# Optimization experiments

Hardware: AMD Instinct MI355X
Metric: run time of the kernel (lower is better)

Reference implementation:

```python
import jax, jax.numpy as jnp
import numpy as np

LAYER_NUMS = 3
# activations per layer: elu, elu, none (matches expert_activations=["elu","elu",null])
ACTS = [jax.nn.elu, jax.nn.elu, None]


def setup_inputs() -> dict:
    key = jax.random.key(0)
    k1, k2, k3, k4 = jax.random.split(key, 4)
    E, D, B_ = 8, 2048, 4096
    weight_blend = jax.random.uniform(k1, (E,), dtype=jnp.float32)
    x = jax.random.normal(k2, (B_, D), dtype=jnp.float32)
    W = jax.random.normal(k3, (LAYER_NUMS, E, D, D), dtype=jnp.float32) * 0.02
    B = jax.random.normal(k4, (LAYER_NUMS, D), dtype=jnp.float32) * 0.02
    return {"weight_blend": weight_blend, "x": x, "W": W, "B": B}


def reference(weight_blend, x, W, B):
    # Dropout is identity in eval/deterministic mode (expert_keep_prob=0.0).
    for i in range(LAYER_NUMS):
        # blended weight: sum_e c_e * W_e  -> (out, in)
        w = jnp.einsum("e,eoi->oi", weight_blend, W[i])
        x = x @ w.T + B[i]
        if ACTS[i] is not None:
            x = ACTS[i](x)
    return x
```

## Files before the change

kernel.cpp:

```cpp
#include <hip/hip_runtime.h>
#include <hip/hip_bf16.h>

#define MDIM 4096
#define NDIM 2048
#define KDIM 2048
#define KTILES 32
#define PER_LAYER 4194304

typedef __attribute__((ext_vector_type(8))) short bf16x8;
typedef __attribute__((ext_vector_type(4))) float f32x4;

__device__ __forceinline__ unsigned short f2bf(float f) {
    unsigned u = __builtin_bit_cast(unsigned, f);
    u += 0x7FFFu + ((u >> 16) & 1u);
    return (unsigned short)(u >> 16);
}

__global__ __launch_bounds__(256) void blend0_kernel(
    const float* __restrict__ W, const float* __restrict__ cb,
    const float* __restrict__ x,
    unsigned short* __restrict__ wb, unsigned short* __restrict__ xb)
{
    float c[8];
#pragma unroll
    for (int e = 0; e < 8; ++e) c[e] = cb[e];
    const unsigned wtotal4 = PER_LAYER >> 2;
    const unsigned xtotal4 = 2097152u;
    const unsigned total = wtotal4 + xtotal4;
    unsigned stride = gridDim.x * blockDim.x;
    for (unsigned i = blockIdx.x * blockDim.x + threadIdx.x; i < total; i += stride) {
        if (i < wtotal4) {
            unsigned off = i << 2;
            const float* base = W + off;
            float4 s = make_float4(0.f, 0.f, 0.f, 0.f);
#pragma unroll
            for (int e = 0; e < 8; ++e) {
                float4 v = *(const float4*)(base + (size_t)e * PER_LAYER);
                s.x += c[e] * v.x; s.y += c[e] * v.y;
                s.z += c[e] * v.z; s.w += c[e] * v.w;
            }
            ushort4 o;
            o.x = f2bf(s.x); o.y = f2bf(s.y); o.z = f2bf(s.z); o.w = f2bf(s.w);
            *(ushort4*)(wb + off) = o;
        } else {
            unsigned j = (i - wtotal4) << 2;
            float4 v = *(const float4*)(x + j);
            ushort4 o;
            o.x = f2bf(v.x); o.y = f2bf(v.y); o.z = f2bf(v.z); o.w = f2bf(v.w);
            *(ushort4*)(xb + j) = o;
        }
    }
}

#define BARR() do { asm volatile("" ::: "memory"); __builtin_amdgcn_s_barrier(); asm volatile("" ::: "memory"); } while (0)
#define SP(N) __builtin_amdgcn_s_setprio(N)
#define VMC_IMPL(N) asm volatile("s_waitcnt vmcnt(" #N ")" ::: "memory")
#define VMC(N) VMC_IMPL(N)

template<int ACT, typename OutT, int BLEND>
__global__ __launch_bounds__(512, 2) void gemm_fused(
    const unsigned short* __restrict__ A,
    const unsigned short* __restrict__ Bw,
    const float* __restrict__ bias,
    OutT* __restrict__ C,
    const float* __restrict__ Wnext,
    const float* __restrict__ cb,
    unsigned short* __restrict__ wbNext)
{
    __shared__ __align__(16) unsigned short lds[73728];
    char* ldsc = (char*)lds;

    const int tid = threadIdx.x;
    const int wid = tid >> 6;
    const int lane = tid & 63;
    const int wr = wid >> 1;
    const int wc = wid & 1;

    float cw[8];
    if (BLEND) {
#pragma unroll
        for (int e = 0; e < 8; ++e) cw[e] = cb[e];
        VMC(0);
    }

    const int wg = (blockIdx.x & 7) * 32 + (blockIdx.x >> 3);
    const size_t blockM = (size_t)(wg & 15) * 256;
    const size_t blockN = (size_t)(wg >> 4) * 128;

    const int sw = (lane & 7) << 4;
    const int ck = (lane >> 4) << 4;
    const int rAb = wr * 64 + (lane & 15);
    const int rBb = wc * 64 + (lane & 15);

    const int srow = tid >> 3;
    const int scol = ((tid & 7) ^ (srow & 7)) << 3;
    const unsigned short* aStage = A + (blockM + srow) * KDIM + scol;
    const unsigned short* bStage = Bw + (blockN + srow) * KDIM + scol;

#define STAGE_AS(BUF, S, KT) do { \
    const unsigned short* g_ = aStage + (size_t)(S) * 64 * KDIM + (size_t)(KT) * 64; \
    __builtin_amdgcn_global_load_lds((const __attribute__((address_space(1))) void*)g_, \
        (__attribute__((address_space(3))) void*)(ldsc + (BUF) * 49152 + (S) * 8192 + tid * 16), \
        16, 0, 0); \
} while (0)

#define STAGE_BS(BUF, S, KT) do { \
    const unsigned short* g_ = bStage + (size_t)(S) * 64 * KDIM + (size_t)(KT) * 64; \
    __builtin_amdgcn_global_load_lds((const __attribute__((address_space(1))) void*)g_, \
        (__attribute__((address_space(3))) void*)(ldsc + (BUF) * 49152 + 32768 + (S) * 8192 + tid * 16), \
        16, 0, 0); \
} while (0)

#define RD_A(BUF, M, KK) \
    (*(const bf16x8*)(ldsc + (BUF) * 49152 + ((rAb + (M) * 16)) * 128 + (((KK) * 64 + ck) ^ sw)))
#define RD_B(BUF, N, KK) \
    (*(const bf16x8*)(ldsc + (BUF) * 49152 + 32768 + (rBb + (N) * 16) * 128 + (((KK) * 64 + ck) ^ sw)))

    f32x4 acc[4][4];
#pragma unroll
    for (int m = 0; m < 4; ++m)
#pragma unroll
        for (int n = 0; n < 4; ++n) acc[m][n] = (f32x4){0.f, 0.f, 0.f, 0.f};

#define GEMM_ITER(T, WAITER) do { \
    int stb_ = cur + 2; if (stb_ >= 3) stb_ -= 3; \
    bf16x8 af[4][2], bfr[4][2]; \
    _Pragma("unroll") for (int m_ = 0; m_ < 4; ++m_) { \
        af[m_][0] = RD_A(cur, m_, 0); af[m_][1] = RD_A(cur, m_, 1); } \
    _Pragma("unroll") for (int n_ = 0; n_ < 4; ++n_) { \
        bfr[n_][0] = RD_B(cur, n_, 0); bfr[n_][1] = RD_B(cur, n_, 1); } \
    if ((T) + 2 < KTILES) { \
        STAGE_AS(stb_, 0, (T) + 2); STAGE_AS(stb_, 1, (T) + 2); \
        STAGE_AS(stb_, 2, (T) + 2); STAGE_AS(stb_, 3, (T) + 2); \
        STAGE_BS(stb_, 0, (T) + 2); STAGE_BS(stb_, 1, (T) + 2); \
    } \
    SP(1); \
    _Pragma("unroll") for (int kk_ = 0; kk_ < 2; ++kk_) \
    _Pragma("unroll") for (int m_ = 0; m_ < 4; ++m_) \
    _Pragma("unroll") for (int n_ = 0; n_ < 4; ++n_) \
        acc[m_][n_] = __builtin_amdgcn_mfma_f32_16x16x32_bf16( \
            af[m_][kk_], bfr[n_][kk_], acc[m_][n_], 0, 0, 0); \
    SP(0); \
    WAITER; \
    BARR(); \
    cur = cur + 1; if (cur >= 3) cur = 0; \
} while (0)

#define BLEND_STEP(G) do { \
    const unsigned idx_ = (unsigned)(G) * 131072u + (unsigned)blockIdx.x * 512u + (unsigned)tid; \
    const unsigned off_ = idx_ << 2; \
    const float* bs_ = Wnext + off_; \
    float4 s_ = make_float4(0.f, 0.f, 0.f, 0.f); \
    _Pragma("unroll") for (int e_ = 0; e_ < 8; ++e_) { \
        float4 v_ = *(const float4*)(bs_ + (size_t)e_ * PER_LAYER); \
        s_.x += cw[e_] * v_.x; s_.y += cw[e_] * v_.y; \
        s_.z += cw[e_] * v_.z; s_.w += cw[e_] * v_.w; } \
    ushort4 o_; \
    o_.x = f2bf(s_.x); o_.y = f2bf(s_.y); o_.z = f2bf(s_.z); o_.w = f2bf(s_.w); \
    *(ushort4*)(wbNext + off_) = o_; \
} while (0)

    STAGE_AS(0, 0, 0); STAGE_AS(0, 1, 0); STAGE_AS(0, 2, 0); STAGE_AS(0, 3, 0);
    STAGE_BS(0, 0, 0); STAGE_BS(0, 1, 0);
    STAGE_AS(1, 0, 1); STAGE_AS(1, 1, 1); STAGE_AS(1, 2, 1); STAGE_AS(1, 3, 1);
    STAGE_BS(1, 0, 1); STAGE_BS(1, 1, 1);
    VMC(6);
    BARR();

    int cur = 0;
    if (BLEND) {
#pragma unroll 1
        for (int g = 0; g < 8; ++g) {
            const int t0 = 3 * g;
            GEMM_ITER(t0, VMC(6));
            BLEND_STEP(g);
            GEMM_ITER(t0 + 1, VMC(15));
            GEMM_ITER(t0 + 2, VMC(6));
        }
#pragma unroll 1
        for (int t = 24; t < 30; ++t) GEMM_ITER(t, VMC(6));
    } else {
#pragma unroll 1
        for (int t = 0; t < 30; ++t) GEMM_ITER(t, VMC(6));
    }
    GEMM_ITER(30, VMC(0));
    GEMM_ITER(31, VMC(0));

    const int crow = (lane >> 4) * 4;
    const int ccol = lane & 15;
#pragma unroll
    for (int m = 0; m < 4; ++m)
#pragma unroll
        for (int n = 0; n < 4; ++n) {
            const size_t col = blockN + wc * 64 + n * 16 + ccol;
            const float bv = bias[col];
#pragma unroll
            for (int r = 0; r < 4; ++r) {
                const size_t row = blockM + wr * 64 + m * 16 + crow + r;
                float v = acc[m][n][r] + bv;
                if (ACT) v = v > 0.f ? v : expm1f(v);
                if constexpr (sizeof(OutT) == 2) {
                    C[row * NDIM + col] = (OutT)f2bf(v);
                } else {
                    C[row * NDIM + col] = (OutT)v;
                }
            }
        }
#undef STAGE_AS
#undef STAGE_BS
#undef RD_A
#undef RD_B
#undef GEMM_ITER
#undef BLEND_STEP
}

extern "C" void kernel_launch(void* const* d_in, const int* in_sizes, int n_in,
                              void* d_out, int out_size, void* d_ws, size_t ws_size,
                              hipStream_t stream) {
    const float* blendw = (const float*)d_in[0];
    const float* x      = (const float*)d_in[1];
    const float* W      = (const float*)d_in[2];
    const float* Bb     = (const float*)d_in[3];
    float* out = (float*)d_out;

    unsigned short* wb0 = (unsigned short*)d_ws;
    unsigned short* wb1 = wb0 + PER_LAYER;
    unsigned short* wb2 = wb1 + PER_LAYER;
    unsigned short* xb  = wb2 + PER_LAYER;
    unsigned short* y0  = xb + 8388608;
    unsigned short* y1  = xb;

    blend0_kernel<<<2048, 256, 0, stream>>>(W, blendw, x, wb0, xb);

    gemm_fused<1, unsigned short, 1><<<256, 512, 0, stream>>>(
        xb, wb0, Bb,        y0,  W + (size_t)8 * PER_LAYER,  blendw, wb1);
    gemm_fused<1, unsigned short, 1><<<256, 512, 0, stream>>>(
        y0, wb1, Bb + 2048, y1,  W + (size_t)16 * PER_LAYER, blendw, wb2);
    gemm_fused<0, float, 0><<<256, 512, 0, stream>>>(
        y1, wb2, Bb + 4096, out, nullptr, nullptr, nullptr);
}
```

Baseline: 204.8 us.

## Shrink GEMM tiles to 128x128 with 256 threads and double buffering

```diff
diff --git a/kernel.cpp b/kernel.cpp
--- a/kernel.cpp
+++ b/kernel.cpp
@@ -58,7 +58,7 @@
 #define VMC(N) VMC_IMPL(N)
 
 template<int ACT, typename OutT, int BLEND>
-__global__ __launch_bounds__(512, 2) void gemm_fused(
+__global__ __launch_bounds__(256, 2) void gemm_fused(
     const unsigned short* __restrict__ A,
     const unsigned short* __restrict__ Bw,
     const float* __restrict__ bias,
@@ -67,7 +67,7 @@
     const float* __restrict__ cb,
     unsigned short* __restrict__ wbNext)
 {
-    __shared__ __align__(16) unsigned short lds[73728];
+    __shared__ __align__(16) unsigned short lds[32768];
     char* ldsc = (char*)lds;
 
     const int tid = threadIdx.x;
@@ -83,9 +83,10 @@
         VMC(0);
     }
 
-    const int wg = (blockIdx.x & 7) * 32 + (blockIdx.x >> 3);
-    const size_t blockM = (size_t)(wg & 15) * 256;
-    const size_t blockN = (size_t)(wg >> 4) * 128;
+    const int k8 = blockIdx.x & 7;
+    const int j = blockIdx.x >> 3;
+    const size_t blockM = (size_t)((k8 & 3) * 8 + (j >> 3)) * 128;
+    const size_t blockN = (size_t)((k8 >> 2) * 8 + (j & 7)) * 128;
 
     const int sw = (lane & 7) << 4;
     const int ck = (lane >> 4) << 4;
@@ -97,24 +98,25 @@
     const unsigned short* aStage = A + (blockM + srow) * KDIM + scol;
     const unsigned short* bStage = Bw + (blockN + srow) * KDIM + scol;
 
-#define STAGE_AS(BUF, S, KT) do { \
-    const unsigned short* g_ = aStage + (size_t)(S) * 64 * KDIM + (size_t)(KT) * 64; \
-    __builtin_amdgcn_global_load_lds((const __attribute__((address_space(1))) void*)g_, \
-        (__attribute__((address_space(3))) void*)(ldsc + (BUF) * 49152 + (S) * 8192 + tid * 16), \
-        16, 0, 0); \
+#define STAGE_TILE(BUF, KT) do { \
+    _Pragma("unroll") for (int s_ = 0; s_ < 4; ++s_) { \
+        const unsigned short* ga_ = aStage + (size_t)s_ * 32 * KDIM + (size_t)(KT) * 64; \
+        __builtin_amdgcn_global_load_lds((const __attribute__((address_space(1))) void*)ga_, \
+            (__attribute__((address_space(3))) void*)(ldsc + (BUF) * 32768 + s_ * 4096 + tid * 16), \
+            16, 0, 0); \
+    } \
+    _Pragma("unroll") for (int s_ = 0; s_ < 4; ++s_) { \
+        const unsigned short* gb_ = bStage + (size_t)s_ * 32 * KDIM + (size_t)(KT) * 64; \
+        __builtin_amdgcn_global_load_lds((const __attribute__((address_space(1))) void*)gb_, \
+            (__attribute__((address_space(3))) void*)(ldsc + (BUF) * 32768 + 16384 + s_ * 4096 + tid * 16), \
+            16, 0, 0); \
+    } \
 } while (0)
 
-#define STAGE_BS(BUF, S, KT) do { \
-    const unsigned short* g_ = bStage + (size_t)(S) * 64 * KDIM + (size_t)(KT) * 64; \
-    __builtin_amdgcn_global_load_lds((const __attribute__((address_space(1))) void*)g_, \
-        (__attribute__((address_space(3))) void*)(ldsc + (BUF) * 49152 + 32768 + (S) * 8192 + tid * 16), \
-        16, 0, 0); \
-} while (0)
-
 #define RD_A(BUF, M, KK) \
-    (*(const bf16x8*)(ldsc + (BUF) * 49152 + ((rAb + (M) * 16)) * 128 + (((KK) * 64 + ck) ^ sw)))
+    (*(const bf16x8*)(ldsc + (BUF) * 32768 + (rAb + (M) * 16) * 128 + (((KK) * 64 + ck) ^ sw)))
 #define RD_B(BUF, N, KK) \
-    (*(const bf16x8*)(ldsc + (BUF) * 49152 + 32768 + (rBb + (N) * 16) * 128 + (((KK) * 64 + ck) ^ sw)))
+    (*(const bf16x8*)(ldsc + (BUF) * 32768 + 16384 + (rBb + (N) * 16) * 128 + (((KK) * 64 + ck) ^ sw)))
 
     f32x4 acc[4][4];
 #pragma unroll
@@ -122,32 +124,8 @@
 #pragma unroll
         for (int n = 0; n < 4; ++n) acc[m][n] = (f32x4){0.f, 0.f, 0.f, 0.f};
 
-#define GEMM_ITER(T, WAITER) do { \
-    int stb_ = cur + 2; if (stb_ >= 3) stb_ -= 3; \
-    bf16x8 af[4][2], bfr[4][2]; \
-    _Pragma("unroll") for (int m_ = 0; m_ < 4; ++m_) { \
-        af[m_][0] = RD_A(cur, m_, 0); af[m_][1] = RD_A(cur, m_, 1); } \
-    _Pragma("unroll") for (int n_ = 0; n_ < 4; ++n_) { \
-        bfr[n_][0] = RD_B(cur, n_, 0); bfr[n_][1] = RD_B(cur, n_, 1); } \
-    if ((T) + 2 < KTILES) { \
-        STAGE_AS(stb_, 0, (T) + 2); STAGE_AS(stb_, 1, (T) + 2); \
-        STAGE_AS(stb_, 2, (T) + 2); STAGE_AS(stb_, 3, (T) + 2); \
-        STAGE_BS(stb_, 0, (T) + 2); STAGE_BS(stb_, 1, (T) + 2); \
-    } \
-    SP(1); \
-    _Pragma("unroll") for (int kk_ = 0; kk_ < 2; ++kk_) \
-    _Pragma("unroll") for (int m_ = 0; m_ < 4; ++m_) \
-    _Pragma("unroll") for (int n_ = 0; n_ < 4; ++n_) \
-        acc[m_][n_] = __builtin_amdgcn_mfma_f32_16x16x32_bf16( \
-            af[m_][kk_], bfr[n_][kk_], acc[m_][n_], 0, 0, 0); \
-    SP(0); \
-    WAITER; \
-    BARR(); \
-    cur = cur + 1; if (cur >= 3) cur = 0; \
-} while (0)
-
 #define BLEND_STEP(G) do { \
-    const unsigned idx_ = (unsigned)(G) * 131072u + (unsigned)blockIdx.x * 512u + (unsigned)tid; \
+    const unsigned idx_ = (unsigned)(G) * 131072u + (unsigned)blockIdx.x * 256u + (unsigned)tid; \
     const unsigned off_ = idx_ << 2; \
     const float* bs_ = Wnext + off_; \
     float4 s_ = make_float4(0.f, 0.f, 0.f, 0.f); \
@@ -160,31 +138,34 @@
     *(ushort4*)(wbNext + off_) = o_; \
 } while (0)
 
-    STAGE_AS(0, 0, 0); STAGE_AS(0, 1, 0); STAGE_AS(0, 2, 0); STAGE_AS(0, 3, 0);
-    STAGE_BS(0, 0, 0); STAGE_BS(0, 1, 0);
-    STAGE_AS(1, 0, 1); STAGE_AS(1, 1, 1); STAGE_AS(1, 2, 1); STAGE_AS(1, 3, 1);
-    STAGE_BS(1, 0, 1); STAGE_BS(1, 1, 1);
-    VMC(6);
+    STAGE_TILE(0, 0);
+    STAGE_TILE(1, 1);
+    VMC(8);
     BARR();
 
-    int cur = 0;
-    if (BLEND) {
 #pragma unroll 1
-        for (int g = 0; g < 8; ++g) {
-            const int t0 = 3 * g;
-            GEMM_ITER(t0, VMC(6));
-            BLEND_STEP(g);
-            GEMM_ITER(t0 + 1, VMC(15));
-            GEMM_ITER(t0 + 2, VMC(6));
-        }
-#pragma unroll 1
-        for (int t = 24; t < 30; ++t) GEMM_ITER(t, VMC(6));
-    } else {
-#pragma unroll 1
-        for (int t = 0; t < 30; ++t) GEMM_ITER(t, VMC(6));
+    for (int t = 0; t < KTILES; ++t) {
+        const int cur = t & 1;
+        bf16x8 af[4][2], bfr[4][2];
+#pragma unroll
+        for (int m = 0; m < 4; ++m) { af[m][0] = RD_A(cur, m, 0); af[m][1] = RD_A(cur, m, 1); }
+#pragma unroll
+        for (int n = 0; n < 4; ++n) { bfr[n][0] = RD_B(cur, n, 0); bfr[n][1] = RD_B(cur, n, 1); }
+        if (t >= 1 && t + 1 < KTILES) STAGE_TILE(cur ^ 1, t + 1);
+        if (BLEND && (t & 3) == 0) BLEND_STEP(t >> 2);
+        SP(1);
+#pragma unroll
+        for (int kk = 0; kk < 2; ++kk)
+#pragma unroll
+            for (int m = 0; m < 4; ++m)
+#pragma unroll
+                for (int n = 0; n < 4; ++n)
+                    acc[m][n] = __builtin_amdgcn_mfma_f32_16x16x32_bf16(
+                        af[m][kk], bfr[n][kk], acc[m][n], 0, 0, 0);
+        SP(0);
+        VMC(0);
+        BARR();
     }
-    GEMM_ITER(30, VMC(0));
-    GEMM_ITER(31, VMC(0));
 
     const int crow = (lane >> 4) * 4;
     const int ccol = lane & 15;
@@ -206,11 +187,9 @@
                 }
             }
         }
-#undef STAGE_AS
-#undef STAGE_BS
+#undef STAGE_TILE
 #undef RD_A
 #undef RD_B
-#undef GEMM_ITER
 #undef BLEND_STEP
 }
 
@@ -232,10 +211,11 @@
 
     blend0_kernel<<<2048, 256, 0, stream>>>(W, blendw, x, wb0, xb);
 
-    gemm_fused<1, unsigned short, 1><<<256, 512, 0, stream>>>(
+    const int grid = (MDIM / 128) * (NDIM / 128);
+    gemm_fused<1, unsigned short, 1><<<grid, 256, 0, stream>>>(
         xb, wb0, Bb,        y0,  W + (size_t)8 * PER_LAYER,  blendw, wb1);
-    gemm_fused<1, unsigned short, 1><<<256, 512, 0, stream>>>(
+    gemm_fused<1, unsigned short, 1><<<grid, 256, 0, stream>>>(
         y0, wb1, Bb + 2048, y1,  W + (size_t)16 * PER_LAYER, blendw, wb2);
-    gemm_fused<0, float, 0><<<256, 512, 0, stream>>>(
+    gemm_fused<0, float, 0><<<grid, 256, 0, stream>>>(
         y1, wb2, Bb + 4096, out, nullptr, nullptr, nullptr);
 }
```

Result: no change. 206.0 us (+0.6%).

## Split GEMM iteration into quadrant phases interleaving LDS reads, staging and MFMA

Applied to the files above, without the earlier changes.

```diff
diff --git a/kernel.cpp b/kernel.cpp
--- a/kernel.cpp
+++ b/kernel.cpp
@@ -54,6 +54,7 @@
 
 #define BARR() do { asm volatile("" ::: "memory"); __builtin_amdgcn_s_barrier(); asm volatile("" ::: "memory"); } while (0)
 #define SP(N) __builtin_amdgcn_s_setprio(N)
+#define LGKM0() asm volatile("s_waitcnt lgkmcnt(0)" ::: "memory")
 #define VMC_IMPL(N) asm volatile("s_waitcnt vmcnt(" #N ")" ::: "memory")
 #define VMC(N) VMC_IMPL(N)
 
@@ -116,35 +117,24 @@
 #define RD_B(BUF, N, KK) \
     (*(const bf16x8*)(ldsc + (BUF) * 49152 + 32768 + (rBb + (N) * 16) * 128 + (((KK) * 64 + ck) ^ sw)))
 
+#define READ_AQ(DST, BUF, MB) do { \
+    DST[0][0] = RD_A(BUF, (MB) + 0, 0); DST[0][1] = RD_A(BUF, (MB) + 0, 1); \
+    DST[1][0] = RD_A(BUF, (MB) + 1, 0); DST[1][1] = RD_A(BUF, (MB) + 1, 1); } while (0)
+#define READ_BQ(DST, BUF, NB) do { \
+    DST[0][0] = RD_B(BUF, (NB) + 0, 0); DST[0][1] = RD_B(BUF, (NB) + 0, 1); \
+    DST[1][0] = RD_B(BUF, (NB) + 1, 0); DST[1][1] = RD_B(BUF, (NB) + 1, 1); } while (0)
+#define MFQ(AQ, BQ, MB, NB) do { \
+    _Pragma("unroll") for (int kk_ = 0; kk_ < 2; ++kk_) \
+    _Pragma("unroll") for (int mi_ = 0; mi_ < 2; ++mi_) \
+    _Pragma("unroll") for (int ni_ = 0; ni_ < 2; ++ni_) \
+        acc[(MB) + mi_][(NB) + ni_] = __builtin_amdgcn_mfma_f32_16x16x32_bf16( \
+            AQ[mi_][kk_], BQ[ni_][kk_], acc[(MB) + mi_][(NB) + ni_], 0, 0, 0); } while (0)
+
     f32x4 acc[4][4];
 #pragma unroll
     for (int m = 0; m < 4; ++m)
 #pragma unroll
         for (int n = 0; n < 4; ++n) acc[m][n] = (f32x4){0.f, 0.f, 0.f, 0.f};
-
-#define GEMM_ITER(T, WAITER) do { \
-    int stb_ = cur + 2; if (stb_ >= 3) stb_ -= 3; \
-    bf16x8 af[4][2], bfr[4][2]; \
-    _Pragma("unroll") for (int m_ = 0; m_ < 4; ++m_) { \
-        af[m_][0] = RD_A(cur, m_, 0); af[m_][1] = RD_A(cur, m_, 1); } \
-    _Pragma("unroll") for (int n_ = 0; n_ < 4; ++n_) { \
-        bfr[n_][0] = RD_B(cur, n_, 0); bfr[n_][1] = RD_B(cur, n_, 1); } \
-    if ((T) + 2 < KTILES) { \
-        STAGE_AS(stb_, 0, (T) + 2); STAGE_AS(stb_, 1, (T) + 2); \
-        STAGE_AS(stb_, 2, (T) + 2); STAGE_AS(stb_, 3, (T) + 2); \
-        STAGE_BS(stb_, 0, (T) + 2); STAGE_BS(stb_, 1, (T) + 2); \
-    } \
-    SP(1); \
-    _Pragma("unroll") for (int kk_ = 0; kk_ < 2; ++kk_) \
-    _Pragma("unroll") for (int m_ = 0; m_ < 4; ++m_) \
-    _Pragma("unroll") for (int n_ = 0; n_ < 4; ++n_) \
-        acc[m_][n_] = __builtin_amdgcn_mfma_f32_16x16x32_bf16( \
-            af[m_][kk_], bfr[n_][kk_], acc[m_][n_], 0, 0, 0); \
-    SP(0); \
-    WAITER; \
-    BARR(); \
-    cur = cur + 1; if (cur >= 3) cur = 0; \
-} while (0)
 
 #define BLEND_STEP(G) do { \
     const unsigned idx_ = (unsigned)(G) * 131072u + (unsigned)blockIdx.x * 512u + (unsigned)tid; \
@@ -160,6 +150,28 @@
     *(ushort4*)(wbNext + off_) = o_; \
 } while (0)
 
+#define GEMM_ITER(T, WAITER) do { \
+    int stb_ = cur + 2; if (stb_ >= 3) stb_ -= 3; \
+    bf16x8 a0_[2][2], a1_[2][2], b0_[2][2], b1_[2][2]; \
+     \
+    READ_AQ(a0_, cur, 0); READ_BQ(b0_, cur, 0); \
+    if ((T) + 2 < KTILES) { STAGE_AS(stb_, 0, (T) + 2); STAGE_AS(stb_, 1, (T) + 2); } \
+    BARR(); LGKM0(); SP(1); MFQ(a0_, b0_, 0, 0); SP(0); BARR(); \
+     \
+    READ_BQ(b1_, cur, 2); \
+    if ((T) + 2 < KTILES) { STAGE_AS(stb_, 2, (T) + 2); STAGE_AS(stb_, 3, (T) + 2); } \
+    BARR(); LGKM0(); SP(1); MFQ(a0_, b1_, 0, 2); SP(0); BARR(); \
+     \
+    READ_AQ(a1_, cur, 2); \
+    if ((T) + 2 < KTILES) { STAGE_BS(stb_, 0, (T) + 2); STAGE_BS(stb_, 1, (T) + 2); } \
+    BARR(); LGKM0(); SP(1); MFQ(a1_, b1_, 2, 2); SP(0); BARR(); \
+     \
+    SP(1); MFQ(a1_, b0_, 2, 0); SP(0); \
+    WAITER; \
+    BARR(); \
+    cur = cur + 1; if (cur >= 3) cur = 0; \
+} while (0)
+
     STAGE_AS(0, 0, 0); STAGE_AS(0, 1, 0); STAGE_AS(0, 2, 0); STAGE_AS(0, 3, 0);
     STAGE_BS(0, 0, 0); STAGE_BS(0, 1, 0);
     STAGE_AS(1, 0, 1); STAGE_AS(1, 1, 1); STAGE_AS(1, 2, 1); STAGE_AS(1, 3, 1);
@@ -171,11 +183,10 @@
     if (BLEND) {
 #pragma unroll 1
         for (int g = 0; g < 8; ++g) {
-            const int t0 = 3 * g;
-            GEMM_ITER(t0, VMC(6));
+            GEMM_ITER(3 * g, VMC(6));
             BLEND_STEP(g);
-            GEMM_ITER(t0 + 1, VMC(15));
-            GEMM_ITER(t0 + 2, VMC(6));
+            GEMM_ITER(3 * g + 1, VMC(15));
+            GEMM_ITER(3 * g + 2, VMC(6));
         }
 #pragma unroll 1
         for (int t = 24; t < 30; ++t) GEMM_ITER(t, VMC(6));
@@ -210,6 +221,9 @@
 #undef STAGE_BS
 #undef RD_A
 #undef RD_B
+#undef READ_AQ
+#undef READ_BQ
+#undef MFQ
 #undef GEMM_ITER
 #undef BLEND_STEP
 }
@@ -232,10 +246,11 @@
 
     blend0_kernel<<<2048, 256, 0, stream>>>(W, blendw, x, wb0, xb);
 
-    gemm_fused<1, unsigned short, 1><<<256, 512, 0, stream>>>(
+    const int grid = (MDIM / 256) * (NDIM / 128);
+    gemm_fused<1, unsigned short, 1><<<grid, 512, 0, stream>>>(
         xb, wb0, Bb,        y0,  W + (size_t)8 * PER_LAYER,  blendw, wb1);
-    gemm_fused<1, unsigned short, 1><<<256, 512, 0, stream>>>(
+    gemm_fused<1, unsigned short, 1><<<grid, 512, 0, stream>>>(
         y0, wb1, Bb + 2048, y1,  W + (size_t)16 * PER_LAYER, blendw, wb2);
-    gemm_fused<0, float, 0><<<256, 512, 0, stream>>>(
+    gemm_fused<0, float, 0><<<grid, 512, 0, stream>>>(
         y1, wb2, Bb + 4096, out, nullptr, nullptr, nullptr);
 }
```

Measured after the change: 207.6 us. No clear change (+1.3%).

## Use 16-wave 1024-thread workgroups with a 4x4 warp grid for GEMM

Applied to the files above, without the earlier changes.

```diff
diff --git a/kernel.cpp b/kernel.cpp
--- a/kernel.cpp
+++ b/kernel.cpp
@@ -58,7 +58,7 @@
 #define VMC(N) VMC_IMPL(N)
 
 template<int ACT, typename OutT, int BLEND>
-__global__ __launch_bounds__(512, 2) void gemm_fused(
+__global__ __launch_bounds__(1024) void gemm_w16(
     const unsigned short* __restrict__ A,
     const unsigned short* __restrict__ Bw,
     const float* __restrict__ bias,
@@ -73,8 +73,8 @@
     const int tid = threadIdx.x;
     const int wid = tid >> 6;
     const int lane = tid & 63;
-    const int wr = wid >> 1;
-    const int wc = wid & 1;
+    const int wr = wid >> 2;
+    const int wc = wid & 3;
 
     float cw[8];
     if (BLEND) {
@@ -90,56 +90,54 @@
     const int sw = (lane & 7) << 4;
     const int ck = (lane >> 4) << 4;
     const int rAb = wr * 64 + (lane & 15);
-    const int rBb = wc * 64 + (lane & 15);
+    const int rBb = wc * 32 + (lane & 15);
 
     const int srow = tid >> 3;
     const int scol = ((tid & 7) ^ (srow & 7)) << 3;
     const unsigned short* aStage = A + (blockM + srow) * KDIM + scol;
     const unsigned short* bStage = Bw + (blockN + srow) * KDIM + scol;
 
-#define STAGE_AS(BUF, S, KT) do { \
-    const unsigned short* g_ = aStage + (size_t)(S) * 64 * KDIM + (size_t)(KT) * 64; \
+#define STAGE_A(BUF, S, KT) do { \
+    const unsigned short* g_ = aStage + (size_t)(S) * 128 * KDIM + (size_t)(KT) * 64; \
     __builtin_amdgcn_global_load_lds((const __attribute__((address_space(1))) void*)g_, \
-        (__attribute__((address_space(3))) void*)(ldsc + (BUF) * 49152 + (S) * 8192 + tid * 16), \
+        (__attribute__((address_space(3))) void*)(ldsc + (BUF) * 49152 + (S) * 16384 + tid * 16), \
         16, 0, 0); \
 } while (0)
 
-#define STAGE_BS(BUF, S, KT) do { \
-    const unsigned short* g_ = bStage + (size_t)(S) * 64 * KDIM + (size_t)(KT) * 64; \
+#define STAGE_B(BUF, KT) do { \
+    const unsigned short* g_ = bStage + (size_t)(KT) * 64; \
     __builtin_amdgcn_global_load_lds((const __attribute__((address_space(1))) void*)g_, \
-        (__attribute__((address_space(3))) void*)(ldsc + (BUF) * 49152 + 32768 + (S) * 8192 + tid * 16), \
+        (__attribute__((address_space(3))) void*)(ldsc + (BUF) * 49152 + 32768 + tid * 16), \
         16, 0, 0); \
 } while (0)
 
 #define RD_A(BUF, M, KK) \
-    (*(const bf16x8*)(ldsc + (BUF) * 49152 + ((rAb + (M) * 16)) * 128 + (((KK) * 64 + ck) ^ sw)))
+    (*(const bf16x8*)(ldsc + (BUF) * 49152 + (rAb + (M) * 16) * 128 + (((KK) * 64 + ck) ^ sw)))
 #define RD_B(BUF, N, KK) \
     (*(const bf16x8*)(ldsc + (BUF) * 49152 + 32768 + (rBb + (N) * 16) * 128 + (((KK) * 64 + ck) ^ sw)))
 
-    f32x4 acc[4][4];
+    f32x4 acc[4][2];
 #pragma unroll
     for (int m = 0; m < 4; ++m)
 #pragma unroll
-        for (int n = 0; n < 4; ++n) acc[m][n] = (f32x4){0.f, 0.f, 0.f, 0.f};
+        for (int n = 0; n < 2; ++n) acc[m][n] = (f32x4){0.f, 0.f, 0.f, 0.f};
 
 #define GEMM_ITER(T, WAITER) do { \
     int stb_ = cur + 2; if (stb_ >= 3) stb_ -= 3; \
-    bf16x8 af[4][2], bfr[4][2]; \
+    bf16x8 af[4][2], bf[2][2]; \
     _Pragma("unroll") for (int m_ = 0; m_ < 4; ++m_) { \
         af[m_][0] = RD_A(cur, m_, 0); af[m_][1] = RD_A(cur, m_, 1); } \
-    _Pragma("unroll") for (int n_ = 0; n_ < 4; ++n_) { \
-        bfr[n_][0] = RD_B(cur, n_, 0); bfr[n_][1] = RD_B(cur, n_, 1); } \
+    _Pragma("unroll") for (int n_ = 0; n_ < 2; ++n_) { \
+        bf[n_][0] = RD_B(cur, n_, 0); bf[n_][1] = RD_B(cur, n_, 1); } \
     if ((T) + 2 < KTILES) { \
-        STAGE_AS(stb_, 0, (T) + 2); STAGE_AS(stb_, 1, (T) + 2); \
-        STAGE_AS(stb_, 2, (T) + 2); STAGE_AS(stb_, 3, (T) + 2); \
-        STAGE_BS(stb_, 0, (T) + 2); STAGE_BS(stb_, 1, (T) + 2); \
+        STAGE_A(stb_, 0, (T) + 2); STAGE_A(stb_, 1, (T) + 2); STAGE_B(stb_, (T) + 2); \
     } \
     SP(1); \
     _Pragma("unroll") for (int kk_ = 0; kk_ < 2; ++kk_) \
     _Pragma("unroll") for (int m_ = 0; m_ < 4; ++m_) \
-    _Pragma("unroll") for (int n_ = 0; n_ < 4; ++n_) \
+    _Pragma("unroll") for (int n_ = 0; n_ < 2; ++n_) \
         acc[m_][n_] = __builtin_amdgcn_mfma_f32_16x16x32_bf16( \
-            af[m_][kk_], bfr[n_][kk_], acc[m_][n_], 0, 0, 0); \
+            af[m_][kk_], bf[n_][kk_], acc[m_][n_], 0, 0, 0); \
     SP(0); \
     WAITER; \
     BARR(); \
@@ -147,7 +145,7 @@
 } while (0)
 
 #define BLEND_STEP(G) do { \
-    const unsigned idx_ = (unsigned)(G) * 131072u + (unsigned)blockIdx.x * 512u + (unsigned)tid; \
+    const unsigned idx_ = (unsigned)(G) * 262144u + (unsigned)blockIdx.x * 1024u + (unsigned)tid; \
     const unsigned off_ = idx_ << 2; \
     const float* bs_ = Wnext + off_; \
     float4 s_ = make_float4(0.f, 0.f, 0.f, 0.f); \
@@ -160,28 +158,30 @@
     *(ushort4*)(wbNext + off_) = o_; \
 } while (0)
 
-    STAGE_AS(0, 0, 0); STAGE_AS(0, 1, 0); STAGE_AS(0, 2, 0); STAGE_AS(0, 3, 0);
-    STAGE_BS(0, 0, 0); STAGE_BS(0, 1, 0);
-    STAGE_AS(1, 0, 1); STAGE_AS(1, 1, 1); STAGE_AS(1, 2, 1); STAGE_AS(1, 3, 1);
-    STAGE_BS(1, 0, 1); STAGE_BS(1, 1, 1);
-    VMC(6);
+    STAGE_A(0, 0, 0); STAGE_A(0, 1, 0); STAGE_B(0, 0);
+    STAGE_A(1, 0, 1); STAGE_A(1, 1, 1); STAGE_B(1, 1);
+    VMC(3);
     BARR();
 
     int cur = 0;
     if (BLEND) {
 #pragma unroll 1
-        for (int g = 0; g < 8; ++g) {
-            const int t0 = 3 * g;
-            GEMM_ITER(t0, VMC(6));
+        for (int g = 0; g < 4; ++g) {
+            GEMM_ITER(8 * g, VMC(3));
             BLEND_STEP(g);
-            GEMM_ITER(t0 + 1, VMC(15));
-            GEMM_ITER(t0 + 2, VMC(6));
+            GEMM_ITER(8 * g + 1, VMC(12));
+            GEMM_ITER(8 * g + 2, VMC(3));
+            GEMM_ITER(8 * g + 3, VMC(3));
+            GEMM_ITER(8 * g + 4, VMC(3));
+            GEMM_ITER(8 * g + 5, VMC(3));
+            if (g < 3) {
+                GEMM_ITER(8 * g + 6, VMC(3));
+                GEMM_ITER(8 * g + 7, VMC(3));
+            }
         }
-#pragma unroll 1
-        for (int t = 24; t < 30; ++t) GEMM_ITER(t, VMC(6));
     } else {
 #pragma unroll 1
-        for (int t = 0; t < 30; ++t) GEMM_ITER(t, VMC(6));
+        for (int t = 0; t < 30; ++t) GEMM_ITER(t, VMC(3));
     }
     GEMM_ITER(30, VMC(0));
     GEMM_ITER(31, VMC(0));
@@ -191,8 +191,8 @@
 #pragma unroll
     for (int m = 0; m < 4; ++m)
 #pragma unroll
-        for (int n = 0; n < 4; ++n) {
-            const size_t col = blockN + wc * 64 + n * 16 + ccol;
+        for (int n = 0; n < 2; ++n) {
+            const size_t col = blockN + wc * 32 + n * 16 + ccol;
             const float bv = bias[col];
 #pragma unroll
             for (int r = 0; r < 4; ++r) {
@@ -206,8 +206,8 @@
                 }
             }
         }
-#undef STAGE_AS
-#undef STAGE_BS
+#undef STAGE_A
+#undef STAGE_B
 #undef RD_A
 #undef RD_B
 #undef GEMM_ITER
@@ -232,10 +232,11 @@
 
     blend0_kernel<<<2048, 256, 0, stream>>>(W, blendw, x, wb0, xb);
 
-    gemm_fused<1, unsigned short, 1><<<256, 512, 0, stream>>>(
+    const int grid = (MDIM / 256) * (NDIM / 128);
+    gemm_w16<1, unsigned short, 1><<<grid, 1024, 0, stream>>>(
         xb, wb0, Bb,        y0,  W + (size_t)8 * PER_LAYER,  blendw, wb1);
-    gemm_fused<1, unsigned short, 1><<<256, 512, 0, stream>>>(
+    gemm_w16<1, unsigned short, 1><<<grid, 1024, 0, stream>>>(
         y0, wb1, Bb + 2048, y1,  W + (size_t)16 * PER_LAYER, blendw, wb2);
-    gemm_fused<0, float, 0><<<256, 512, 0, stream>>>(
+    gemm_w16<0, float, 0><<<grid, 1024, 0, stream>>>(
         y1, wb2, Bb + 4096, out, nullptr, nullptr, nullptr);
 }
```

Result: slower. 210.2 us (+2.6%).
